# Kernel optimization log

Hardware: AMD Instinct MI355X
Metric: run time of the kernel (lower is better)

Reference implementation:

```python
import jax, jax.numpy as jnp
import numpy as np

B, S, D, H = 2, 2048, 1024, 16
HD = D // H  # head_dim = 64


def setup_inputs() -> dict:
    key = jax.random.key(0)
    ks = jax.random.split(key, 5)
    scale = 0.02
    x = jax.random.normal(ks[0], (B, S, D), dtype=jnp.float32)
    Wq = scale * jax.random.normal(ks[1], (H, D, HD), dtype=jnp.float32)
    Wk = scale * jax.random.normal(ks[2], (H, D, HD), dtype=jnp.float32)
    Wv = scale * jax.random.normal(ks[3], (H, D, HD), dtype=jnp.float32)
    Wo = scale * jax.random.normal(ks[4], (D, D), dtype=jnp.float32)
    bq = jnp.zeros((H, HD), dtype=jnp.float32)
    bk = jnp.zeros((H, HD), dtype=jnp.float32)
    bv = jnp.zeros((H, HD), dtype=jnp.float32)
    bo = jnp.zeros((D,), dtype=jnp.float32)
    return {"x": x, "Wq": Wq, "bq": bq, "Wk": Wk, "bk": bk,
            "Wv": Wv, "bv": bv, "Wo": Wo, "bo": bo}


def reference(x, Wq, bq, Wk, bk, Wv, bv, Wo, bo):
    # Per-head QKV projections (the torch module's per-head nn.Linear list,
    # vectorized over the head axis h). Dropout is identity (eval mode).
    q = jnp.einsum("bsd,hde->bhse", x, Wq) + bq[None, :, None, :]  # [B,H,S,HD]
    k = jnp.einsum("bsd,hde->bhse", x, Wk) + bk[None, :, None, :]
    v = jnp.einsum("bsd,hde->bhse", x, Wv) + bv[None, :, None, :]

    norm = jnp.asarray(np.sqrt(HD), dtype=x.dtype)
    scores = jnp.einsum("bhse,bhte->bhst", q, k) / norm  # [B,H,S,S]
    causal = jnp.tril(jnp.ones((S, S), dtype=bool))
    scores = jnp.where(causal[None, None], scores, jnp.asarray(-jnp.inf, dtype=scores.dtype))
    attn = jax.nn.softmax(scores, axis=-1)

    wv = jnp.einsum("bhst,bhte->bhse", attn, v)          # [B,H,S,HD]
    wv = jnp.transpose(wv, (0, 2, 1, 3)).reshape(B, S, D)  # concat heads on last dim
    out = wv @ Wo.T + bo                                   # output projection
    return out
```

## Files before the change

kernel.cpp:

```cpp
#include <hip/hip_runtime.h>


#define DD 1024
#define SS 2048
#define BB 2
#define HH 16
#define HD 64
#define QSCALE 0.18033688011112042f

typedef __attribute__((ext_vector_type(8))) short short8;
typedef __attribute__((ext_vector_type(4))) float float4v;
typedef unsigned short ushort;
typedef unsigned int uint;

__device__ inline ushort f2bf(float f) {
    union { float f; uint i; } v; v.f = f;
    uint r = v.i + 0x7FFF + ((v.i >> 16) & 1);
    return (ushort)(r >> 16);
}
#if __has_builtin(__builtin_amdgcn_cvt_pk_bf16_f32)
typedef __bf16 bf16x2 __attribute__((ext_vector_type(2)));
__device__ inline uint pack_bf2(float a, float b) {
    union { bf16x2 v; uint u; } c;
    c.v = __builtin_amdgcn_cvt_pk_bf16_f32(a, b);
    return c.u;
}
#else
__device__ inline uint pack_bf2(float a, float b) {
    union { float f; uint i; } x, y; x.f = a; y.f = b;
    return ((x.i + 0x8000u) >> 16) | (((y.i + 0x8000u) >> 16) << 16);
}
#endif

__device__ __forceinline__ void cp16(const ushort* g, ushort* l) {
    __builtin_amdgcn_global_load_lds((const __attribute__((address_space(1))) void*)g,
                                     (__attribute__((address_space(3))) void*)l,
                                     16, 0, 0);
}

__global__ __launch_bounds__(256) void prep(const float* __restrict__ x,
                                            const float* __restrict__ Wo,
                                            const float* __restrict__ Wq,
                                            const float* __restrict__ Wk,
                                            const float* __restrict__ Wv,
                                            ushort* __restrict__ xb,
                                            ushort* __restrict__ Wob,
                                            ushort* __restrict__ W3T) {
    __shared__ ushort T[64][65];
    int bid = blockIdx.x, t = threadIdx.x;
    if (bid < 5120) {
        const float* src; ushort* dst; int j;
        if (bid < 4096) { src = x;  dst = xb;  j = bid * 256 + t; }
        else            { src = Wo; dst = Wob; j = (bid - 4096) * 256 + t; }
        float4 v = ((const float4*)src)[j];
        ushort o[4] = { f2bf(v.x), f2bf(v.y), f2bf(v.z), f2bf(v.w) };
        ((uint2*)dst)[j] = *(const uint2*)o;
        return;
    }
    int i = bid - 5120;
    int z = i >> 8, h = (i >> 4) & 15, d0 = (i & 15) * 64;
    const float* W = z == 0 ? Wq : (z == 1 ? Wk : Wv);
    const float* Wh = W + h * DD * HD;
    ushort* Wt = W3T + ((size_t)z * HH + h) * HD * DD;
    #pragma unroll
    for (int s = 0; s < 4; s++) {
        int idx = t + s * 256;
        int d = idx >> 4, e4 = (idx & 15) * 4;
        float4 v = *(const float4*)(Wh + (d0 + d) * HD + e4);
        T[d][e4 + 0] = f2bf(v.x); T[d][e4 + 1] = f2bf(v.y);
        T[d][e4 + 2] = f2bf(v.z); T[d][e4 + 3] = f2bf(v.w);
    }
    __syncthreads();
    #pragma unroll
    for (int s = 0; s < 2; s++) {
        int idx = t + s * 256;
        int e = idx >> 3, d8 = (idx & 7) * 8;
        ushort tmp[8];
        #pragma unroll
        for (int j = 0; j < 8; j++) tmp[j] = T[d8 + j][e];
        *(uint4*)(Wt + e * DD + d0 + d8) = *(uint4*)tmp;
    }
}

__global__ __launch_bounds__(256) void gemm_qkv(const ushort* __restrict__ xb,
                                                const ushort* __restrict__ W3T,
                                                const float* __restrict__ bq,
                                                const float* __restrict__ bk,
                                                const float* __restrict__ bv,
                                                ushort* __restrict__ qb,
                                                ushort* __restrict__ kb,
                                                ushort* __restrict__ vT) {
    __shared__ ushort Al[128 * 64];
    __shared__ ushort Bl[3][64 * 64];
    int m0 = blockIdx.x * 128, n0 = blockIdx.y * 64;
    int t = threadIdx.x, lane = t & 63, w = t >> 6;
    int wm = w & 1, wn = w >> 1;
    int qm = lane >> 4, lm = lane & 15;

    const ushort* W0 = W3T + (size_t)n0 * DD;
    const ushort* W1 = W3T + (size_t)(HH * HD + n0) * DD;
    const ushort* W2 = W3T + (size_t)(2 * HH * HD + n0) * DD;

    float4v acc[3][4][2] = {};
    for (int k0 = 0; k0 < DD; k0 += 64) {
        __syncthreads();
        #pragma unroll
        for (int s = 0; s < 4; s++) {
            int c = t + s * 256;
            int row = c >> 3;
            int j = (c & 7) ^ (row & 7);
            cp16(xb + (size_t)(m0 + row) * DD + k0 + j * 8, Al + c * 8);
        }
        #pragma unroll
        for (int s = 0; s < 2; s++) {
            int c = t + s * 256;
            int row = c >> 3;
            int j = (c & 7) ^ (row & 7);
            cp16(W0 + (size_t)row * DD + k0 + j * 8, Bl[0] + c * 8);
            cp16(W1 + (size_t)row * DD + k0 + j * 8, Bl[1] + c * 8);
            cp16(W2 + (size_t)row * DD + k0 + j * 8, Bl[2] + c * 8);
        }
        __syncthreads();
        #pragma unroll
        for (int h2 = 0; h2 < 2; h2++) {
            int sw = ((((h2 << 2) | qm) ^ (lm & 7)) << 3);
            short8 a[4];
            #pragma unroll
            for (int i = 0; i < 4; i++)
                a[i] = *(const short8*)(Al + ((wm * 64 + i * 16 + lm) << 6) + sw);
            #pragma unroll
            for (int z = 0; z < 3; z++) {
                short8 b0 = *(const short8*)(Bl[z] + ((wn * 32 + lm) << 6) + sw);
                short8 b1 = *(const short8*)(Bl[z] + ((wn * 32 + 16 + lm) << 6) + sw);
                if (z == 2) {
                    #pragma unroll
                    for (int i = 0; i < 4; i++) {
                        acc[2][i][0] = __builtin_amdgcn_mfma_f32_16x16x32_bf16(a[i], b0, acc[2][i][0], 0, 0, 0);
                        acc[2][i][1] = __builtin_amdgcn_mfma_f32_16x16x32_bf16(a[i], b1, acc[2][i][1], 0, 0, 0);
                    }
                } else {
                    #pragma unroll
                    for (int i = 0; i < 4; i++) {
                        acc[z][i][0] = __builtin_amdgcn_mfma_f32_16x16x32_bf16(b0, a[i], acc[z][i][0], 0, 0, 0);
                        acc[z][i][1] = __builtin_amdgcn_mfma_f32_16x16x32_bf16(b1, a[i], acc[z][i][1], 0, 0, 0);
                    }
                }
            }
        }
    }
    #pragma unroll
    for (int z = 0; z < 2; z++) {
        const float* bias = z == 0 ? bq : bk;
        ushort* Out = z == 0 ? qb : kb;
        float sc = z == 0 ? QSCALE : 1.0f;
        #pragma unroll
        for (int j = 0; j < 2; j++) {
            int nb = n0 + wn * 32 + j * 16 + qm * 4;
            float4 b4 = *(const float4*)(bias + nb);
            #pragma unroll
            for (int i = 0; i < 4; i++) {
                int m = m0 + wm * 64 + i * 16 + lm;
                uint2 o2;
                o2.x = pack_bf2((acc[z][i][j][0] + b4.x) * sc, (acc[z][i][j][1] + b4.y) * sc);
                o2.y = pack_bf2((acc[z][i][j][2] + b4.z) * sc, (acc[z][i][j][3] + b4.w) * sc);
                *(uint2*)(Out + (size_t)m * DD + nb) = o2;
            }
        }
    }
    #pragma unroll
    for (int j = 0; j < 2; j++) {
        int n = n0 + wn * 32 + j * 16 + lm;
        int h = n >> 6, e = n & 63;
        float bb = bv[n];
        #pragma unroll
        for (int i = 0; i < 4; i++) {
            int m = m0 + wm * 64 + i * 16 + qm * 4;
            int b_ = m >> 11, s = m & (SS - 1);
            uint2 o2;
            o2.x = pack_bf2(acc[2][i][j][0] + bb, acc[2][i][j][1] + bb);
            o2.y = pack_bf2(acc[2][i][j][2] + bb, acc[2][i][j][3] + bb);
            *(uint2*)(vT + ((size_t)(b_ * HH + h) * HD + e) * SS + s) = o2;
        }
    }
}

__global__ __launch_bounds__(128, 2) void attn(const ushort* __restrict__ Q,
                                               const ushort* __restrict__ K,
                                               const ushort* __restrict__ VT,
                                               ushort* __restrict__ O) {
    __shared__ ushort Ql[64 * 64];
    __shared__ ushort Kl[2][64 * 64];
    __shared__ ushort Vl[2][64 * 64];
    int id = blockIdx.x;
    int bh = id & 31;
    int j5 = (id >> 5) & 7;
    int quad = id >> 8;
    int qt = (quad == 0) ? (31 - j5) : (quad == 1) ? (16 + j5)
           : (quad == 2) ? (15 - j5) : j5;
    int b = bh >> 4, h = bh & 15;
    int m0 = qt * 64;
    const ushort* Qp = Q + (size_t)b * SS * DD + h * HD;
    const ushort* Kp = K + (size_t)b * SS * DD + h * HD;
    const ushort* Vp = VT + (size_t)bh * HD * SS;
    int t = threadIdx.x, lane = t & 63, w = t >> 6;
    int qm = lane >> 4, lm = lane & 15;
    int swz = ((qm ^ (lm & 7)) << 3);
    int swz1 = (((4 | qm) ^ (lm & 7)) << 3);

    #pragma unroll
    for (int s2 = 0; s2 < 4; s2++) {
        int c = t + s2 * 128;
        int row = c >> 3, sj = (c & 7) ^ (row & 7);
        cp16(Qp + (size_t)(m0 + row) * DD + sj * 8, Ql + c * 8);
        cp16(Kp + (size_t)row * DD + sj * 8, Kl[0] + c * 8);
        cp16(Vp + (size_t)row * SS + sj * 8, Vl[0] + c * 8);
    }
    __syncthreads();

    short8 qf[2][2];
    #pragma unroll
    for (int g = 0; g < 2; g++) {
        int rb = (w * 32 + g * 16 + lm) << 6;
        qf[g][0] = *(const short8*)(Ql + rb + swz);
        qf[g][1] = *(const short8*)(Ql + rb + swz1);
    }

    float4v o[4][2] = {};
    float li[2] = {0.f, 0.f};
    int cur = 0;

    for (int jt = 0; jt <= qt; jt++) {
        if (jt) __syncthreads();
        if (jt < qt) {
            int nn = (jt + 1) * 64;
            #pragma unroll
            for (int s2 = 0; s2 < 4; s2++) {
                int c = t + s2 * 128;
                int row = c >> 3, sj = (c & 7) ^ (row & 7);
                cp16(Kp + (size_t)(nn + row) * DD + sj * 8, Kl[cur ^ 1] + c * 8);
                cp16(Vp + (size_t)row * SS + nn + sj * 8, Vl[cur ^ 1] + c * 8);
            }
        }

        float4v s[4][2] = {};
        __builtin_amdgcn_s_setprio(1);
        #pragma unroll
        for (int j = 0; j < 4; j++) {
            short8 ak0 = *(const short8*)(Kl[cur] + ((j * 16 + lm) << 6) + swz);
            short8 ak1 = *(const short8*)(Kl[cur] + ((j * 16 + lm) << 6) + swz1);
            #pragma unroll
            for (int g = 0; g < 2; g++) {
                s[j][g] = __builtin_amdgcn_mfma_f32_16x16x32_bf16(ak0, qf[g][0], s[j][g], 0, 0, 0);
                s[j][g] = __builtin_amdgcn_mfma_f32_16x16x32_bf16(ak1, qf[g][1], s[j][g], 0, 0, 0);
            }
        }
        __builtin_amdgcn_s_setprio(0);
        if (jt == qt) {
            #pragma unroll
            for (int g = 0; g < 2; g++) {
                int qg = m0 + w * 32 + g * 16 + lm;
                #pragma unroll
                for (int j = 0; j < 4; j++)
                    #pragma unroll
                    for (int r = 0; r < 4; r++)
                        if (jt * 64 + j * 16 + qm * 4 + r > qg) s[j][g][r] = -__builtin_inff();
            }
        }
        #pragma unroll
        for (int g = 0; g < 2; g++) {
            int rb = (w * 32 + g * 16 + lm) << 6;
            #pragma unroll
            for (int j = 0; j < 4; j++) {
                float p0 = __builtin_amdgcn_exp2f(s[j][g][0]);
                float p1 = __builtin_amdgcn_exp2f(s[j][g][1]);
                float p2 = __builtin_amdgcn_exp2f(s[j][g][2]);
                float p3 = __builtin_amdgcn_exp2f(s[j][g][3]);
                li[g] += (p0 + p1) + (p2 + p3);
                uint2 u; u.x = pack_bf2(p0, p1); u.y = pack_bf2(p2, p3);
                int pc = (2 * j + (qm >> 1)) ^ (lm & 7);
                *(uint2*)(Ql + rb + (pc << 3) + (qm & 1) * 4) = u;
            }
        }
        asm volatile("s_waitcnt lgkmcnt(0)" ::: "memory");

        __builtin_amdgcn_s_setprio(1);
        #pragma unroll
        for (int kc = 0; kc < 2; kc++) {
            short8 ap[2];
            #pragma unroll
            for (int g = 0; g < 2; g++)
                ap[g] = *(const short8*)(Ql + ((w * 32 + g * 16 + lm) << 6) + (kc ? swz1 : swz));
            #pragma unroll
            for (int jn = 0; jn < 4; jn++) {
                short8 av = *(const short8*)(Vl[cur] + ((jn * 16 + lm) << 6) + (kc ? swz1 : swz));
                #pragma unroll
                for (int g = 0; g < 2; g++)
                    o[jn][g] = __builtin_amdgcn_mfma_f32_16x16x32_bf16(av, ap[g], o[jn][g], 0, 0, 0);
            }
        }
        __builtin_amdgcn_s_setprio(0);
        cur ^= 1;
    }
    #pragma unroll
    for (int g = 0; g < 2; g++) {
        float l = li[g];
        l += __shfl_xor(l, 16, 64);
        l += __shfl_xor(l, 32, 64);
        float inv = 1.f / l;
        int qg = m0 + w * 32 + g * 16 + lm;
        ushort* Ob = O + ((size_t)b * SS + qg) * DD + h * HD;
        #pragma unroll
        for (int jn = 0; jn < 4; jn++) {
            uint2 u;
            u.x = pack_bf2(o[jn][g][0] * inv, o[jn][g][1] * inv);
            u.y = pack_bf2(o[jn][g][2] * inv, o[jn][g][3] * inv);
            *(uint2*)(Ob + jn * 16 + qm * 4) = u;
        }
    }
}

__global__ __launch_bounds__(256) void gemm_out(const ushort* __restrict__ X,
                                                const ushort* __restrict__ Wob,
                                                const float* __restrict__ bo,
                                                float* __restrict__ Out) {
    __shared__ ushort Al[128 * 64];
    __shared__ ushort Bl[64 * 64];
    int m0 = blockIdx.x * 128, n0 = blockIdx.y * 64;
    int t = threadIdx.x, lane = t & 63, w = t >> 6;
    int wm = w & 1, wn = w >> 1;
    int qm = lane >> 4, lm = lane & 15;

    float4v acc[4][2] = {};
    for (int k0 = 0; k0 < DD; k0 += 64) {
        __syncthreads();
        #pragma unroll
        for (int s = 0; s < 4; s++) {
            int c = t + s * 256;
            int row = c >> 3;
            int j = (c & 7) ^ (row & 7);
            cp16(X + (size_t)(m0 + row) * DD + k0 + j * 8, Al + c * 8);
        }
        #pragma unroll
        for (int s = 0; s < 2; s++) {
            int c = t + s * 256;
            int row = c >> 3;
            int j = (c & 7) ^ (row & 7);
            cp16(Wob + (size_t)(n0 + row) * DD + k0 + j * 8, Bl + c * 8);
        }
        __syncthreads();
        #pragma unroll
        for (int h2 = 0; h2 < 2; h2++) {
            int sw = ((((h2 << 2) | qm) ^ (lm & 7)) << 3);
            short8 a[4], b[2];
            #pragma unroll
            for (int i = 0; i < 4; i++)
                a[i] = *(const short8*)(Al + ((wm * 64 + i * 16 + lm) << 6) + sw);
            #pragma unroll
            for (int j = 0; j < 2; j++)
                b[j] = *(const short8*)(Bl + ((wn * 32 + j * 16 + lm) << 6) + sw);
            #pragma unroll
            for (int i = 0; i < 4; i++)
                #pragma unroll
                for (int j = 0; j < 2; j++)
                    acc[i][j] = __builtin_amdgcn_mfma_f32_16x16x32_bf16(b[j], a[i], acc[i][j], 0, 0, 0);
        }
    }
    #pragma unroll
    for (int j = 0; j < 2; j++) {
        int nb = n0 + wn * 32 + j * 16 + qm * 4;
        float4 b4 = *(const float4*)(bo + nb);
        #pragma unroll
        for (int i = 0; i < 4; i++) {
            int m = m0 + wm * 64 + i * 16 + lm;
            float4 st;
            st.x = acc[i][j][0] + b4.x;
            st.y = acc[i][j][1] + b4.y;
            st.z = acc[i][j][2] + b4.z;
            st.w = acc[i][j][3] + b4.w;
            *(float4*)(Out + (size_t)m * DD + nb) = st;
        }
    }
}

extern "C" void kernel_launch(void* const* d_in, const int* in_sizes, int n_in,
                              void* d_out, int out_size, void* d_ws, size_t ws_size,
                              hipStream_t stream) {
    const float* x   = (const float*)d_in[0];
    const float* Wq  = (const float*)d_in[1];
    const float* bq  = (const float*)d_in[2];
    const float* Wk  = (const float*)d_in[3];
    const float* bk  = (const float*)d_in[4];
    const float* Wv_ = (const float*)d_in[5];
    const float* bv  = (const float*)d_in[6];
    const float* Wo  = (const float*)d_in[7];
    const float* bo  = (const float*)d_in[8];
    float* out = (float*)d_out;

    ushort* xb  = (ushort*)d_ws;
    ushort* W3T = xb  + (size_t)BB * SS * DD;
    ushort* Wob = W3T + (size_t)3 * HH * HD * DD;
    ushort* qb  = Wob + (size_t)DD * DD;
    ushort* kb  = qb + (size_t)BB * SS * DD;
    ushort* vT  = kb + (size_t)BB * SS * DD;
    ushort* wvb = vT + (size_t)BB * SS * DD;

    prep<<<dim3(5888), 256, 0, stream>>>(x, Wo, Wq, Wk, Wv_, xb, Wob, W3T);
    gemm_qkv<<<dim3(32, 16), 256, 0, stream>>>(xb, W3T, bq, bk, bv, qb, kb, vT);
    attn<<<dim3(1024), 128, 0, stream>>>(qb, kb, vT, wvb);
    gemm_out<<<dim3(32, 16), 256, 0, stream>>>(wvb, Wob, bo, out);
}
```

Before: 187.7 us.

## Split attention KV tiles across two wave pairs and reduce partial outputs

The attention kernel now launches 256 threads per block. The block has two wave pairs, and each pair processes alternating 64-key tiles for the same 64-query tile. Partial outputs and row sums from the second pair are combined through LDS at the end. This doubles the waves working on each query tile to cut per-block latency on the causal diagonal. The cost is extra LDS traffic for the reduction, two barriers per step instead of overlapped double buffering, and loads no longer prefetched ahead of compute. Because softmax uses no running max (plain exp2 of pre-scaled scores), the partial results can simply be added.

```diff
diff --git a/kernel.cpp b/kernel.cpp
--- a/kernel.cpp
+++ b/kernel.cpp
@@ -184,13 +184,12 @@
     }
 }
 
-__global__ __launch_bounds__(128, 2) void attn(const ushort* __restrict__ Q,
+__global__ __launch_bounds__(256, 3) void attn(const ushort* __restrict__ Q,
                                                const ushort* __restrict__ K,
                                                const ushort* __restrict__ VT,
                                                ushort* __restrict__ O) {
-    __shared__ ushort Ql[64 * 64];
-    __shared__ ushort Kl[2][64 * 64];
-    __shared__ ushort Vl[2][64 * 64];
+    __shared__ ushort LB[24576];
+    ushort* QP = LB;
     int id = blockIdx.x;
     int bh = id & 31;
     int j5 = (id >> 5) & 7;
@@ -203,118 +202,163 @@
     const ushort* Kp = K + (size_t)b * SS * DD + h * HD;
     const ushort* Vp = VT + (size_t)bh * HD * SS;
     int t = threadIdx.x, lane = t & 63, w = t >> 6;
+    int pr = w >> 1, wq = w & 1;
     int qm = lane >> 4, lm = lane & 15;
     int swz = ((qm ^ (lm & 7)) << 3);
     int swz1 = (((4 | qm) ^ (lm & 7)) << 3);
-
-    #pragma unroll
-    for (int s2 = 0; s2 < 4; s2++) {
-        int c = t + s2 * 128;
-        int row = c >> 3, sj = (c & 7) ^ (row & 7);
-        cp16(Qp + (size_t)(m0 + row) * DD + sj * 8, Ql + c * 8);
-        cp16(Kp + (size_t)row * DD + sj * 8, Kl[0] + c * 8);
-        cp16(Vp + (size_t)row * SS + sj * 8, Vl[0] + c * 8);
+    int c0 = t, c1 = t + 256;
+    int r0 = c0 >> 3, s0 = (c0 & 7) ^ (r0 & 7);
+    int r1 = c1 >> 3, s1 = (c1 & 7) ^ (r1 & 7);
+
+    cp16(Qp + (size_t)(m0 + r0) * DD + s0 * 8, QP + c0 * 8);
+    cp16(Qp + (size_t)(m0 + r1) * DD + s1 * 8, QP + c1 * 8);
+    cp16(Kp + (size_t)r0 * DD + s0 * 8, LB + 8192 + c0 * 8);
+    cp16(Kp + (size_t)r1 * DD + s1 * 8, LB + 8192 + c1 * 8);
+    cp16(Vp + (size_t)r0 * SS + s0 * 8, LB + 12288 + c0 * 8);
+    cp16(Vp + (size_t)r1 * SS + s1 * 8, LB + 12288 + c1 * 8);
+    if (qt >= 1) {
+        cp16(Kp + (size_t)(64 + r0) * DD + s0 * 8, LB + 16384 + c0 * 8);
+        cp16(Kp + (size_t)(64 + r1) * DD + s1 * 8, LB + 16384 + c1 * 8);
+        cp16(Vp + (size_t)r0 * SS + 64 + s0 * 8, LB + 20480 + c0 * 8);
+        cp16(Vp + (size_t)r1 * SS + 64 + s1 * 8, LB + 20480 + c1 * 8);
     }
     __syncthreads();
 
     short8 qf[2][2];
     #pragma unroll
     for (int g = 0; g < 2; g++) {
-        int rb = (w * 32 + g * 16 + lm) << 6;
-        qf[g][0] = *(const short8*)(Ql + rb + swz);
-        qf[g][1] = *(const short8*)(Ql + rb + swz1);
-    }
-
+        int rb = (wq * 32 + g * 16 + lm) << 6;
+        qf[g][0] = *(const short8*)(QP + rb + swz);
+        qf[g][1] = *(const short8*)(QP + rb + swz1);
+    }
+    __syncthreads();
+
+    ushort* Kb = LB + 8192 + pr * 8192;
+    ushort* Vb = LB + 12288 + pr * 8192;
     float4v o[4][2] = {};
     float li[2] = {0.f, 0.f};
-    int cur = 0;
-
-    for (int jt = 0; jt <= qt; jt++) {
-        if (jt) __syncthreads();
-        if (jt < qt) {
-            int nn = (jt + 1) * 64;
-            #pragma unroll
-            for (int s2 = 0; s2 < 4; s2++) {
-                int c = t + s2 * 128;
-                int row = c >> 3, sj = (c & 7) ^ (row & 7);
-                cp16(Kp + (size_t)(nn + row) * DD + sj * 8, Kl[cur ^ 1] + c * 8);
-                cp16(Vp + (size_t)row * SS + nn + sj * 8, Vl[cur ^ 1] + c * 8);
-            }
-        }
-
-        float4v s[4][2] = {};
-        __builtin_amdgcn_s_setprio(1);
-        #pragma unroll
-        for (int j = 0; j < 4; j++) {
-            short8 ak0 = *(const short8*)(Kl[cur] + ((j * 16 + lm) << 6) + swz);
-            short8 ak1 = *(const short8*)(Kl[cur] + ((j * 16 + lm) << 6) + swz1);
+    int nss = (qt + 2) >> 1;
+
+    for (int ss = 0; ss < nss; ss++) {
+        int myjt = 2 * ss + pr;
+        if (myjt <= qt) {
+            float4v s[4][2] = {};
+            __builtin_amdgcn_s_setprio(1);
+            #pragma unroll
+            for (int j = 0; j < 4; j++) {
+                short8 ak0 = *(const short8*)(Kb + ((j * 16 + lm) << 6) + swz);
+                short8 ak1 = *(const short8*)(Kb + ((j * 16 + lm) << 6) + swz1);
+                #pragma unroll
+                for (int g = 0; g < 2; g++) {
+                    s[j][g] = __builtin_amdgcn_mfma_f32_16x16x32_bf16(ak0, qf[g][0], s[j][g], 0, 0, 0);
+                    s[j][g] = __builtin_amdgcn_mfma_f32_16x16x32_bf16(ak1, qf[g][1], s[j][g], 0, 0, 0);
+                }
+            }
+            __builtin_amdgcn_s_setprio(0);
+            if (myjt == qt) {
+                #pragma unroll
+                for (int g = 0; g < 2; g++) {
+                    int qg = m0 + wq * 32 + g * 16 + lm;
+                    #pragma unroll
+                    for (int j = 0; j < 4; j++)
+                        #pragma unroll
+                        for (int r = 0; r < 4; r++)
+                            if (myjt * 64 + j * 16 + qm * 4 + r > qg) s[j][g][r] = -__builtin_inff();
+                }
+            }
             #pragma unroll
             for (int g = 0; g < 2; g++) {
-                s[j][g] = __builtin_amdgcn_mfma_f32_16x16x32_bf16(ak0, qf[g][0], s[j][g], 0, 0, 0);
-                s[j][g] = __builtin_amdgcn_mfma_f32_16x16x32_bf16(ak1, qf[g][1], s[j][g], 0, 0, 0);
-            }
-        }
-        __builtin_amdgcn_s_setprio(0);
-        if (jt == qt) {
+                int rb = (w * 32 + g * 16 + lm) << 6;
+                #pragma unroll
+                for (int j = 0; j < 4; j++) {
+                    float p0 = __builtin_amdgcn_exp2f(s[j][g][0]);
+                    float p1 = __builtin_amdgcn_exp2f(s[j][g][1]);
+                    float p2 = __builtin_amdgcn_exp2f(s[j][g][2]);
+                    float p3 = __builtin_amdgcn_exp2f(s[j][g][3]);
+                    li[g] += (p0 + p1) + (p2 + p3);
+                    uint2 u; u.x = pack_bf2(p0, p1); u.y = pack_bf2(p2, p3);
+                    int pc = (2 * j + (qm >> 1)) ^ (lm & 7);
+                    *(uint2*)(QP + rb + (pc << 3) + (qm & 1) * 4) = u;
+                }
+            }
+            asm volatile("s_waitcnt lgkmcnt(0)" ::: "memory");
+
+            __builtin_amdgcn_s_setprio(1);
+            #pragma unroll
+            for (int kc = 0; kc < 2; kc++) {
+                short8 ap[2];
+                #pragma unroll
+                for (int g = 0; g < 2; g++)
+                    ap[g] = *(const short8*)(QP + ((w * 32 + g * 16 + lm) << 6) + (kc ? swz1 : swz));
+                #pragma unroll
+                for (int jn = 0; jn < 4; jn++) {
+                    short8 av = *(const short8*)(Vb + ((jn * 16 + lm) << 6) + (kc ? swz1 : swz));
+                    #pragma unroll
+                    for (int g = 0; g < 2; g++)
+                        o[jn][g] = __builtin_amdgcn_mfma_f32_16x16x32_bf16(av, ap[g], o[jn][g], 0, 0, 0);
+                }
+            }
+            __builtin_amdgcn_s_setprio(0);
+        }
+        __syncthreads();
+        int nx = 2 * ss + 2;
+        if (nx <= qt) {
+            cp16(Kp + (size_t)(nx * 64 + r0) * DD + s0 * 8, LB + 8192 + c0 * 8);
+            cp16(Kp + (size_t)(nx * 64 + r1) * DD + s1 * 8, LB + 8192 + c1 * 8);
+            cp16(Vp + (size_t)r0 * SS + nx * 64 + s0 * 8, LB + 12288 + c0 * 8);
+            cp16(Vp + (size_t)r1 * SS + nx * 64 + s1 * 8, LB + 12288 + c1 * 8);
+        }
+        if (nx + 1 <= qt) {
+            cp16(Kp + (size_t)((nx + 1) * 64 + r0) * DD + s0 * 8, LB + 16384 + c0 * 8);
+            cp16(Kp + (size_t)((nx + 1) * 64 + r1) * DD + s1 * 8, LB + 16384 + c1 * 8);
+            cp16(Vp + (size_t)r0 * SS + (nx + 1) * 64 + s0 * 8, LB + 20480 + c0 * 8);
+            cp16(Vp + (size_t)r1 * SS + (nx + 1) * 64 + s1 * 8, LB + 20480 + c1 * 8);
+        }
+        __syncthreads();
+    }
+
+    float* cb = (float*)(LB + 8192);
+    float* cl = (float*)(LB + 16384);
+    if (pr == 1) {
+        float* dst = cb + ((size_t)(wq * 64 + lane)) * 32;
+        #pragma unroll
+        for (int jn = 0; jn < 4; jn++)
             #pragma unroll
             for (int g = 0; g < 2; g++) {
-                int qg = m0 + w * 32 + g * 16 + lm;
-                #pragma unroll
-                for (int j = 0; j < 4; j++)
-                    #pragma unroll
-                    for (int r = 0; r < 4; r++)
-                        if (jt * 64 + j * 16 + qm * 4 + r > qg) s[j][g][r] = -__builtin_inff();
-            }
-        }
+                int slot = jn * 2 + g;
+                *(float4v*)(dst + ((slot ^ (lane & 7)) << 2)) = o[jn][g];
+            }
+        cl[(wq * 64 + lane) * 2 + 0] = li[0];
+        cl[(wq * 64 + lane) * 2 + 1] = li[1];
+    }
+    __syncthreads();
+    if (pr == 0) {
+        float* src = cb + ((size_t)(wq * 64 + lane)) * 32;
+        #pragma unroll
+        for (int jn = 0; jn < 4; jn++)
+            #pragma unroll
+            for (int g = 0; g < 2; g++) {
+                int slot = jn * 2 + g;
+                float4v v = *(const float4v*)(src + ((slot ^ (lane & 7)) << 2));
+                o[jn][g] += v;
+            }
+        li[0] += cl[(wq * 64 + lane) * 2 + 0];
+        li[1] += cl[(wq * 64 + lane) * 2 + 1];
         #pragma unroll
         for (int g = 0; g < 2; g++) {
-            int rb = (w * 32 + g * 16 + lm) << 6;
-            #pragma unroll
-            for (int j = 0; j < 4; j++) {
-                float p0 = __builtin_amdgcn_exp2f(s[j][g][0]);
-                float p1 = __builtin_amdgcn_exp2f(s[j][g][1]);
-                float p2 = __builtin_amdgcn_exp2f(s[j][g][2]);
-                float p3 = __builtin_amdgcn_exp2f(s[j][g][3]);
-                li[g] += (p0 + p1) + (p2 + p3);
-                uint2 u; u.x = pack_bf2(p0, p1); u.y = pack_bf2(p2, p3);
-                int pc = (2 * j + (qm >> 1)) ^ (lm & 7);
-                *(uint2*)(Ql + rb + (pc << 3) + (qm & 1) * 4) = u;
-            }
-        }
-        asm volatile("s_waitcnt lgkmcnt(0)" ::: "memory");
-
-        __builtin_amdgcn_s_setprio(1);
-        #pragma unroll
-        for (int kc = 0; kc < 2; kc++) {
-            short8 ap[2];
-            #pragma unroll
-            for (int g = 0; g < 2; g++)
-                ap[g] = *(const short8*)(Ql + ((w * 32 + g * 16 + lm) << 6) + (kc ? swz1 : swz));
+            float l = li[g];
+            l += __shfl_xor(l, 16, 64);
+            l += __shfl_xor(l, 32, 64);
+            float inv = 1.f / l;
+            int qg = m0 + wq * 32 + g * 16 + lm;
+            ushort* Ob = O + ((size_t)b * SS + qg) * DD + h * HD;
             #pragma unroll
             for (int jn = 0; jn < 4; jn++) {
-                short8 av = *(const short8*)(Vl[cur] + ((jn * 16 + lm) << 6) + (kc ? swz1 : swz));
-                #pragma unroll
-                for (int g = 0; g < 2; g++)
-                    o[jn][g] = __builtin_amdgcn_mfma_f32_16x16x32_bf16(av, ap[g], o[jn][g], 0, 0, 0);
-            }
-        }
-        __builtin_amdgcn_s_setprio(0);
-        cur ^= 1;
-    }
-    #pragma unroll
-    for (int g = 0; g < 2; g++) {
-        float l = li[g];
-        l += __shfl_xor(l, 16, 64);
-        l += __shfl_xor(l, 32, 64);
-        float inv = 1.f / l;
-        int qg = m0 + w * 32 + g * 16 + lm;
-        ushort* Ob = O + ((size_t)b * SS + qg) * DD + h * HD;
-        #pragma unroll
-        for (int jn = 0; jn < 4; jn++) {
-            uint2 u;
-            u.x = pack_bf2(o[jn][g][0] * inv, o[jn][g][1] * inv);
-            u.y = pack_bf2(o[jn][g][2] * inv, o[jn][g][3] * inv);
-            *(uint2*)(Ob + jn * 16 + qm * 4) = u;
+                uint2 u;
+                u.x = pack_bf2(o[jn][g][0] * inv, o[jn][g][1] * inv);
+                u.y = pack_bf2(o[jn][g][2] * inv, o[jn][g][3] * inv);
+                *(uint2*)(Ob + jn * 16 + qm * 4) = u;
+            }
         }
     }
 }
@@ -406,6 +450,6 @@
 
     prep<<<dim3(5888), 256, 0, stream>>>(x, Wo, Wq, Wk, Wv_, xb, Wob, W3T);
     gemm_qkv<<<dim3(32, 16), 256, 0, stream>>>(xb, W3T, bq, bk, bv, qb, kb, vT);
-    attn<<<dim3(1024), 128, 0, stream>>>(qb, kb, vT, wvb);
+    attn<<<dim3(1024), 256, 0, stream>>>(qb, kb, vT, wvb);
     gemm_out<<<dim3(32, 16), 256, 0, stream>>>(wvb, Wob, bo, out);
 }
```

Result: faster. 175.1 us (-6.7%).
